# Optimization experiments

Measured on AMD Instinct MI355X. Metric: run time of the kernel, lower is better.

Reference implementation:

```python
import jax, jax.numpy as jnp
import numpy as np

N_NODES = 20000
N_EDGES = 500000


def setup_inputs() -> dict:
    key = jax.random.key(0)
    ks = jax.random.split(key, 12)
    s = 0.05  # small init scale for numerical sanity
    return {
        "z": jax.random.normal(ks[0], (N_NODES, 64), jnp.float32),
        "edge_index": jax.random.randint(ks[1], (2, N_EDGES), 0, N_NODES, jnp.int64),
        "celline_feats": jax.random.normal(ks[2], (N_NODES, 4), jnp.float32),
        "esm_repr": jax.random.normal(ks[3], (N_NODES, 320), jnp.float32),
        "mlp_w1": jax.random.normal(ks[4], (4, 64), jnp.float32) * s,
        "mlp_b1": jnp.zeros((64,), jnp.float32),
        "mlp_w2": jax.random.normal(ks[5], (64, 32), jnp.float32) * s,
        "mlp_b2": jnp.zeros((32,), jnp.float32),
        "mlp_w3": jax.random.normal(ks[6], (32, 16), jnp.float32) * s,
        "mlp_b3": jnp.zeros((16,), jnp.float32),
        "fc1_w": jax.random.normal(ks[7], (800, 400), jnp.float32) * s,
        "fc1_b": jnp.zeros((400,), jnp.float32),
        "fc2_w": jax.random.normal(ks[8], (400, 200), jnp.float32) * s,
        "fc2_b": jnp.zeros((200,), jnp.float32),
        "fc3_w": jax.random.normal(ks[9], (200, 100), jnp.float32) * s,
        "fc3_b": jnp.zeros((100,), jnp.float32),
        "fc4_w": jax.random.normal(ks[10], (100, 1), jnp.float32) * s,
        "fc4_b": jnp.zeros((1,), jnp.float32),
    }


def reference(z, edge_index, celline_feats, esm_repr,
              mlp_w1, mlp_b1, mlp_w2, mlp_b2, mlp_w3, mlp_b3,
              fc1_w, fc1_b, fc2_w, fc2_b, fc3_w, fc3_b, fc4_w, fc4_b):
    # cell_line_spec_mlp: 4 -> 64 -> 32 -> 16 (relu, relu, linear)
    m = jax.nn.relu(celline_feats @ mlp_w1 + mlp_b1)
    m = jax.nn.relu(m @ mlp_w2 + mlp_b2)
    m = m @ mlp_w3 + mlp_b3                       # [N, 16]
    # augment node embeddings: [N, 64+16+320] = [N, 400]
    zc = jnp.concatenate([z, m, esm_repr], axis=1)
    # gather endpoints, concat pair features: [E, 800]
    x = jnp.concatenate([zc[edge_index[0]], zc[edge_index[1]]], axis=1)
    # classifier MLP (dropout = identity in eval mode)
    x = jax.nn.relu(x @ fc1_w + fc1_b)
    x = jax.nn.relu(x @ fc2_w + fc2_b)
    x = jax.nn.relu(x @ fc3_w + fc3_b)
    x = x @ fc4_w + fc4_b                          # [E, 1]
    return jnp.squeeze(x, axis=-1)                 # [E]
```

## Files before the change

kernel.cpp:

```cpp
#include <hip/hip_runtime.h>


using u16    = unsigned short;
using bf16x8 = __attribute__((ext_vector_type(8))) short;
using f32x4  = __attribute__((ext_vector_type(4))) float;
using f32x16 = __attribute__((ext_vector_type(16))) float;
using i32x4  = __attribute__((ext_vector_type(4))) int;

#define NN   20000
#define NNP  20032
#define KD   416
#define NE   500000

#define W1F_ELEMS (50*13*512)
#define W2F_ELEMS (7*26*512)
#define W3F_ELEMS (4*14*512)
#define F4_ELEMS  128
#define PREP_TOT  (W1F_ELEMS + W2F_ELEMS + W3F_ELEMS + F4_ELEMS)

#define ZC_BLOCKS   (NNP / 4)
#define PREP_BLOCKS ((PREP_TOT + 255) / 256)

__device__ __forceinline__ u16 f2bf(float f) {
  unsigned u = __float_as_uint(f);
  u += 0x7fffu + ((u >> 16) & 1u);
  return (u16)(u >> 16);
}

__device__ __forceinline__ int cvt_pk_bf16(float lo, float hi) {
  int r;
  asm("v_cvt_pk_bf16_f32 %0, %1, %2" : "=v"(r) : "v"(lo), "v"(hi));
  return r;
}

__device__ __forceinline__ void gl_lds16(const u16* g, u16* l) {
  __builtin_amdgcn_global_load_lds(
      (const __attribute__((address_space(1))) unsigned int*)g,
      (__attribute__((address_space(3))) unsigned int*)l, 16, 0, 0);
}

__global__ __launch_bounds__(256) void prep_fused(
    const float* __restrict__ z, const float* __restrict__ cell,
    const float* __restrict__ esm,
    const float* __restrict__ w1, const float* __restrict__ b1,
    const float* __restrict__ w2, const float* __restrict__ b2,
    const float* __restrict__ w3, const float* __restrict__ b3,
    u16* __restrict__ zc,
    const float* __restrict__ fc1, const float* __restrict__ fc1b,
    const float* __restrict__ fc2, const float* __restrict__ fc2b,
    const float* __restrict__ fc3, const float* __restrict__ fc3b,
    const float* __restrict__ fc4,
    u16* __restrict__ W1f, u16* __restrict__ W2f, u16* __restrict__ W3f,
    float* __restrict__ fc4wp)
{
  __shared__ float h1s[4][64];
  __shared__ float h2s[4][32];
  __shared__ float ms[4][16];

  if (blockIdx.x < ZC_BLOCKS) {
    int tid = threadIdx.x, g = tid >> 6, t = tid & 63;
    int i = blockIdx.x * 4 + g;
    bool real = (i < NN);
    float c0 = 0, c1 = 0, c2 = 0, c3 = 0;
    if (real) {
      c0 = cell[(size_t)i * 4 + 0]; c1 = cell[(size_t)i * 4 + 1];
      c2 = cell[(size_t)i * 4 + 2]; c3 = cell[(size_t)i * 4 + 3];
    }
    float h = b1[t] + c0 * w1[t] + c1 * w1[64 + t] + c2 * w1[128 + t] + c3 * w1[192 + t];
    h1s[g][t] = fmaxf(h, 0.f);
    __syncthreads();
    if (t < 32) {
      float acc = b2[t];
      #pragma unroll 8
      for (int j = 0; j < 64; j++) acc += h1s[g][j] * w2[j * 32 + t];
      h2s[g][t] = fmaxf(acc, 0.f);
    }
    __syncthreads();
    if (t < 16) {
      float acc = b3[t];
      #pragma unroll 8
      for (int j = 0; j < 32; j++) acc += h2s[g][j] * w3[j * 16 + t];
      ms[g][t] = acc;
    }
    __syncthreads();
    u16* row = zc + (size_t)i * KD;
    for (int k = t; k < KD; k += 64) {
      float v = 0.f;
      if (real) {
        if (k < 64)       v = z[(size_t)i * 64 + k];
        else if (k < 80)  v = ms[g][k - 64];
        else if (k < 400) v = esm[(size_t)i * 320 + (k - 80)];
        else if (k == 400) v = 1.0f;
      }
      row[k] = f2bf(v);
    }
    return;
  }

  int idx = (blockIdx.x - ZC_BLOCKS) * 256 + threadIdx.x;
  if (idx < W1F_ELEMS) {
    int j = idx & 7, l = (idx >> 3) & 63, t = idx >> 9;
    int kb = t % 13, g = t / 13;
    int n = g * 16 + (l & 15);
    int k = kb * 32 + (l >> 4) * 8 + j;
    float v = 0.f;
    if (k < 400) v = (n < 400) ? fc1[(size_t)k * 400 + n]
                               : fc1[(size_t)(400 + k) * 400 + (n - 400)];
    else if (k == 400 && n < 400) v = fc1b[n];
    W1f[idx] = f2bf(v);
  } else if (idx < W1F_ELEMS + W2F_ELEMS) {
    int r = idx - W1F_ELEMS;
    int j = r & 7, l = (r >> 3) & 63, t = r >> 9;
    int kb = t % 26, nt = t / 26;
    int n = nt * 32 + (l & 31);
    int k = kb * 16 + (l >> 5) * 8 + j;
    float v = 0.f;
    if (n < 200) {
      if (k < 400) v = fc2[(size_t)k * 200 + n];
      else if (k == 400) v = fc2b[n];
    }
    W2f[r] = f2bf(v);
  } else if (idx < W1F_ELEMS + W2F_ELEMS + W3F_ELEMS) {
    int r = idx - (W1F_ELEMS + W2F_ELEMS);
    int j = r & 7, l = (r >> 3) & 63, t = r >> 9;
    int kb = t % 14, nt = t / 14;
    int n = nt * 32 + (l & 31);
    int k = kb * 16 + (l >> 5) * 8 + j;
    float v = 0.f;
    if (n < 100) {
      if (k < 200) v = fc3[(size_t)k * 100 + n];
      else if (k == 200) v = fc3b[n];
    }
    W3f[r] = f2bf(v);
  } else if (idx < PREP_TOT) {
    int r = idx - (W1F_ELEMS + W2F_ELEMS + W3F_ELEMS);
    fc4wp[r] = (r < 100) ? fc4[r] : 0.f;
  }
}

__global__ __launch_bounds__(256) void node_gemm(
    const u16* __restrict__ zc, const u16* __restrict__ W1f,
    u16* __restrict__ PQ)
{
  int tid = threadIdx.x, w = tid >> 6, l = tid & 63, lm = l & 15, quad = l >> 4;
  int mbase = blockIdx.x * 128 + w * 32;

  int ra = mbase + lm;       if (ra > NNP - 1) ra = NNP - 1;
  int rb = mbase + 16 + lm;  if (rb > NNP - 1) rb = NNP - 1;
  bf16x8 a0[13], a1[13];
  const u16* arow0 = zc + (size_t)ra * KD + quad * 8;
  const u16* arow1 = zc + (size_t)rb * KD + quad * 8;
  #pragma unroll
  for (int kb = 0; kb < 13; kb++) {
    a0[kb] = *(const bf16x8*)(arow0 + kb * 32);
    a1[kb] = *(const bf16x8*)(arow1 + kb * 32);
  }

  for (int nt = 0; nt < 10; nt++) {
    int g = blockIdx.y * 10 + nt;
    int ncol = g * 16 + lm;
    const u16* bbase = W1f + ((size_t)g * 13 * 64 + l) * 8;
    f32x4 acc0 = {0.f, 0.f, 0.f, 0.f};
    f32x4 acc1 = {0.f, 0.f, 0.f, 0.f};
    #pragma unroll
    for (int kb = 0; kb < 13; kb++) {
      bf16x8 b = *(const bf16x8*)(bbase + (size_t)kb * 512);
      acc0 = __builtin_amdgcn_mfma_f32_16x16x32_bf16(a0[kb], b, acc0, 0, 0, 0);
      acc1 = __builtin_amdgcn_mfma_f32_16x16x32_bf16(a1[kb], b, acc1, 0, 0, 0);
    }
    #pragma unroll
    for (int r = 0; r < 4; r++) {
      int row0 = mbase + quad * 4 + r;
      int row1 = row0 + 16;
      if (row0 < NNP) PQ[(size_t)row0 * 800 + ncol] = f2bf(acc0[r]);
      if (row1 < NNP) PQ[(size_t)row1 * 800 + ncol] = f2bf(acc1[r]);
    }
  }
}

__global__ __launch_bounds__(256, 3) void edge_kernel(
    const u16* __restrict__ PQ, const u16* __restrict__ W2f,
    const u16* __restrict__ W3f, const float* __restrict__ fc4wp,
    const float* __restrict__ fc4b,
    const int* __restrict__ ei, float* __restrict__ out)
{
  __shared__ __align__(16) u16 wsm[2][26 * 512];

  int tid = threadIdx.x, w = tid >> 6, l = tid & 63;
  int c = l & 31, h = l >> 5;
  int e = blockIdx.x * 128 + w * 32 + c;
  int ec = e < NE ? e : NE - 1;
  int s = ei[ec], d = ei[NE + ec];
  const u16* prow = PQ + (size_t)s * 800 + h * 8;
  const u16* qrow = PQ + (size_t)d * 800 + 400 + h * 8;

  for (int kb = w; kb < 26; kb += 4)
    gl_lds16(W2f + ((size_t)kb * 64 + l) * 8, &wsm[0][kb * 512]);

  i32x4 h1i[25];
  #pragma unroll
  for (int kb = 0; kb < 25; kb++) {
    i32x4 pv = *(const i32x4*)(prow + kb * 16);
    i32x4 qv = *(const i32x4*)(qrow + kb * 16);
    i32x4 r;
    #pragma unroll
    for (int j2 = 0; j2 < 4; j2++) {
      unsigned pu = (unsigned)pv[j2], qu = (unsigned)qv[j2];
      float lo = __uint_as_float(pu << 16) + __uint_as_float(qu << 16);
      float hi = __uint_as_float(pu & 0xFFFF0000u) + __uint_as_float(qu & 0xFFFF0000u);
      r[j2] = cvt_pk_bf16(fmaxf(lo, 0.f), fmaxf(hi, 0.f));
    }
    h1i[kb] = r;
  }
  i32x4 bias1 = {0, 0, 0, 0};
  if (h == 0) bias1[0] = 0x3f80;

  __syncthreads();

  int p2[7][8];
  #pragma unroll
  for (int nt = 0; nt < 7; nt++) {
    int cur = nt & 1;
    if (nt < 6) {
      for (int kb = w; kb < 26; kb += 4)
        gl_lds16(W2f + (((size_t)(nt + 1) * 26 + kb) * 64 + l) * 8,
                 &wsm[cur ^ 1][kb * 512]);
    } else {
      for (int kb = w; kb < 14; kb += 4)
        gl_lds16(W3f + ((size_t)kb * 64 + l) * 8, &wsm[cur ^ 1][kb * 512]);
    }
    f32x16 acc = {0.f,0.f,0.f,0.f,0.f,0.f,0.f,0.f,0.f,0.f,0.f,0.f,0.f,0.f,0.f,0.f};
    __builtin_amdgcn_s_setprio(1);
    #pragma unroll
    for (int kb = 0; kb < 25; kb++) {
      bf16x8 a = *(const bf16x8*)&wsm[cur][kb * 512 + l * 8];
      acc = __builtin_amdgcn_mfma_f32_32x32x16_bf16(
          a, __builtin_bit_cast(bf16x8, h1i[kb]), acc, 0, 0, 0);
    }
    {
      bf16x8 a = *(const bf16x8*)&wsm[cur][25 * 512 + l * 8];
      acc = __builtin_amdgcn_mfma_f32_32x32x16_bf16(
          a, __builtin_bit_cast(bf16x8, bias1), acc, 0, 0, 0);
    }
    __builtin_amdgcn_s_setprio(0);
    #pragma unroll
    for (int q = 0; q < 8; q++)
      p2[nt][q] = cvt_pk_bf16(fmaxf(acc[2 * q], 0.f), fmaxf(acc[2 * q + 1], 0.f));
    __syncthreads();
  }

  i32x4 b2f[14];
  #pragma unroll
  for (int kb3 = 0; kb3 < 14; kb3++) {
    int nt = kb3 >> 1;
    i32x4 f;
    #pragma unroll
    for (int jj = 0; jj < 4; jj++) {
      int q0 = (jj & 1) + 4 * (kb3 & 1);
      if (jj < 2) {
        int x = __shfl_xor(p2[nt][q0 + 2], 32);
        f[jj] = h ? x : p2[nt][q0];
      } else {
        int y = __shfl_xor(p2[nt][q0], 32);
        f[jj] = h ? p2[nt][q0 + 2] : y;
      }
    }
    if (kb3 == 12 && h) f[0] |= 0x3f80;
    b2f[kb3] = f;
  }

  float osum = 0.f;
  #pragma unroll
  for (int nt3 = 0; nt3 < 4; nt3++) {
    int cur = (7 + nt3) & 1;
    if (nt3 < 3) {
      for (int kb = w; kb < 14; kb += 4)
        gl_lds16(W3f + (((size_t)(nt3 + 1) * 14 + kb) * 64 + l) * 8,
                 &wsm[cur ^ 1][kb * 512]);
    }
    f32x16 acc = {0.f,0.f,0.f,0.f,0.f,0.f,0.f,0.f,0.f,0.f,0.f,0.f,0.f,0.f,0.f,0.f};
    __builtin_amdgcn_s_setprio(1);
    #pragma unroll
    for (int kb3 = 0; kb3 < 14; kb3++) {
      bf16x8 a = *(const bf16x8*)&wsm[cur][kb3 * 512 + l * 8];
      acc = __builtin_amdgcn_mfma_f32_32x32x16_bf16(
          a, __builtin_bit_cast(bf16x8, b2f[kb3]), acc, 0, 0, 0);
    }
    __builtin_amdgcn_s_setprio(0);
    #pragma unroll
    for (int r = 0; r < 16; r++) {
      int rho = (r & 3) + 8 * (r >> 2) + 4 * h + 32 * nt3;
      osum += fmaxf(acc[r], 0.f) * fc4wp[rho];
    }
    if (nt3 < 3) __syncthreads();
  }
  osum += __shfl_xor(osum, 32);
  if (h == 0 && e < NE) out[e] = osum + fc4b[0];
}

extern "C" void kernel_launch(void* const* d_in, const int* in_sizes, int n_in,
                              void* d_out, int out_size, void* d_ws, size_t ws_size,
                              hipStream_t stream) {
  (void)in_sizes; (void)n_in; (void)out_size; (void)ws_size;
  const float* z    = (const float*)d_in[0];
  const int*   ei   = (const int*)d_in[1];
  const float* cell = (const float*)d_in[2];
  const float* esm  = (const float*)d_in[3];
  const float* w1   = (const float*)d_in[4];
  const float* b1   = (const float*)d_in[5];
  const float* w2   = (const float*)d_in[6];
  const float* b2   = (const float*)d_in[7];
  const float* w3   = (const float*)d_in[8];
  const float* b3   = (const float*)d_in[9];
  const float* fc1w = (const float*)d_in[10];
  const float* fc1b = (const float*)d_in[11];
  const float* fc2w = (const float*)d_in[12];
  const float* fc2b = (const float*)d_in[13];
  const float* fc3w = (const float*)d_in[14];
  const float* fc3b = (const float*)d_in[15];
  const float* fc4w = (const float*)d_in[16];
  const float* fc4b = (const float*)d_in[17];
  float* out = (float*)d_out;

  u16* zc  = (u16*)d_ws;
  u16* PQ  = zc  + (size_t)NNP * KD;
  u16* W1f = PQ  + (size_t)NNP * 800;
  u16* W2f = W1f + W1F_ELEMS;
  u16* W3f = W2f + W2F_ELEMS;
  float* fc4wp = (float*)(W3f + W3F_ELEMS);

  prep_fused<<<ZC_BLOCKS + PREP_BLOCKS, 256, 0, stream>>>(
      z, cell, esm, w1, b1, w2, b2, w3, b3, zc,
      fc1w, fc1b, fc2w, fc2b, fc3w, fc3b, fc4w, W1f, W2f, W3f, fc4wp);
  node_gemm<<<dim3((NNP + 127) / 128, 5), 256, 0, stream>>>(zc, W1f, PQ);
  edge_kernel<<<(NE + 127) / 128, 256, 0, stream>>>(PQ, W2f, W3f, fc4wp, fc4b, ei, out);
}
```

Measured before the change: 359.2 us.

## Switch activations and weights from bf16 to fp16 with packed add-relu

Converts all stored activations and weights from bf16 to fp16 and uses fp16 MFMA instructions. The edge gather now does its add and relu with packed v_pk_add_f16/v_pk_max_f16, replacing the per-element unpack/add/convert sequence. The layer-3 K loop drops its all-zero 14th block, and edge_kernel occupancy is lowered from 3 to 2 waves per SIMD so the compiler gets more registers. fp16 has a narrower range than bf16, so large activations could overflow, and fewer resident waves reduces latency hiding.

Measured after the change: 356.8 us. Within noise of the previous version (-0.7%).

```diff
diff --git a/kernel.cpp b/kernel.cpp
--- a/kernel.cpp
+++ b/kernel.cpp
@@ -2,7 +2,8 @@
 
 
 using u16    = unsigned short;
-using bf16x8 = __attribute__((ext_vector_type(8))) short;
+using f16    = _Float16;
+using f16x8  = __attribute__((ext_vector_type(8))) f16;
 using f32x4  = __attribute__((ext_vector_type(4))) float;
 using f32x16 = __attribute__((ext_vector_type(16))) float;
 using i32x4  = __attribute__((ext_vector_type(4))) int;
@@ -21,15 +22,22 @@
 #define ZC_BLOCKS   (NNP / 4)
 #define PREP_BLOCKS ((PREP_TOT + 255) / 256)
 
-__device__ __forceinline__ u16 f2bf(float f) {
-  unsigned u = __float_as_uint(f);
-  u += 0x7fffu + ((u >> 16) & 1u);
-  return (u16)(u >> 16);
-}
-
-__device__ __forceinline__ int cvt_pk_bf16(float lo, float hi) {
+__device__ __forceinline__ u16 f2h(float f) {
+  f16 h = (f16)f;
+  return __builtin_bit_cast(u16, h);
+}
+
+__device__ __forceinline__ int cvt_pk_f16(float lo, float hi) {
   int r;
-  asm("v_cvt_pk_bf16_f32 %0, %1, %2" : "=v"(r) : "v"(lo), "v"(hi));
+  asm("v_cvt_pkrtz_f16_f32 %0, %1, %2" : "=v"(r) : "v"(lo), "v"(hi));
+  return r;
+}
+
+__device__ __forceinline__ int pk_addrelu(int p, int q) {
+  int r;
+  asm("v_pk_add_f16 %0, %1, %2\n\t"
+      "v_pk_max_f16 %0, %0, 0"
+      : "=&v"(r) : "v"(p), "v"(q));
   return r;
 }
 
@@ -92,7 +100,7 @@
         else if (k < 400) v = esm[(size_t)i * 320 + (k - 80)];
         else if (k == 400) v = 1.0f;
       }
-      row[k] = f2bf(v);
+      row[k] = f2h(v);
     }
     return;
   }
@@ -107,7 +115,7 @@
     if (k < 400) v = (n < 400) ? fc1[(size_t)k * 400 + n]
                                : fc1[(size_t)(400 + k) * 400 + (n - 400)];
     else if (k == 400 && n < 400) v = fc1b[n];
-    W1f[idx] = f2bf(v);
+    W1f[idx] = f2h(v);
   } else if (idx < W1F_ELEMS + W2F_ELEMS) {
     int r = idx - W1F_ELEMS;
     int j = r & 7, l = (r >> 3) & 63, t = r >> 9;
@@ -119,7 +127,7 @@
       if (k < 400) v = fc2[(size_t)k * 200 + n];
       else if (k == 400) v = fc2b[n];
     }
-    W2f[r] = f2bf(v);
+    W2f[r] = f2h(v);
   } else if (idx < W1F_ELEMS + W2F_ELEMS + W3F_ELEMS) {
     int r = idx - (W1F_ELEMS + W2F_ELEMS);
     int j = r & 7, l = (r >> 3) & 63, t = r >> 9;
@@ -131,7 +139,7 @@
       if (k < 200) v = fc3[(size_t)k * 100 + n];
       else if (k == 200) v = fc3b[n];
     }
-    W3f[r] = f2bf(v);
+    W3f[r] = f2h(v);
   } else if (idx < PREP_TOT) {
     int r = idx - (W1F_ELEMS + W2F_ELEMS + W3F_ELEMS);
     fc4wp[r] = (r < 100) ? fc4[r] : 0.f;
@@ -147,13 +155,13 @@
 
   int ra = mbase + lm;       if (ra > NNP - 1) ra = NNP - 1;
   int rb = mbase + 16 + lm;  if (rb > NNP - 1) rb = NNP - 1;
-  bf16x8 a0[13], a1[13];
+  f16x8 a0[13], a1[13];
   const u16* arow0 = zc + (size_t)ra * KD + quad * 8;
   const u16* arow1 = zc + (size_t)rb * KD + quad * 8;
   #pragma unroll
   for (int kb = 0; kb < 13; kb++) {
-    a0[kb] = *(const bf16x8*)(arow0 + kb * 32);
-    a1[kb] = *(const bf16x8*)(arow1 + kb * 32);
+    a0[kb] = *(const f16x8*)(arow0 + kb * 32);
+    a1[kb] = *(const f16x8*)(arow1 + kb * 32);
   }
 
   for (int nt = 0; nt < 10; nt++) {
@@ -164,21 +172,21 @@
     f32x4 acc1 = {0.f, 0.f, 0.f, 0.f};
     #pragma unroll
     for (int kb = 0; kb < 13; kb++) {
-      bf16x8 b = *(const bf16x8*)(bbase + (size_t)kb * 512);
-      acc0 = __builtin_amdgcn_mfma_f32_16x16x32_bf16(a0[kb], b, acc0, 0, 0, 0);
-      acc1 = __builtin_amdgcn_mfma_f32_16x16x32_bf16(a1[kb], b, acc1, 0, 0, 0);
+      f16x8 b = *(const f16x8*)(bbase + (size_t)kb * 512);
+      acc0 = __builtin_amdgcn_mfma_f32_16x16x32_f16(a0[kb], b, acc0, 0, 0, 0);
+      acc1 = __builtin_amdgcn_mfma_f32_16x16x32_f16(a1[kb], b, acc1, 0, 0, 0);
     }
     #pragma unroll
     for (int r = 0; r < 4; r++) {
       int row0 = mbase + quad * 4 + r;
       int row1 = row0 + 16;
-      if (row0 < NNP) PQ[(size_t)row0 * 800 + ncol] = f2bf(acc0[r]);
-      if (row1 < NNP) PQ[(size_t)row1 * 800 + ncol] = f2bf(acc1[r]);
-    }
-  }
-}
-
-__global__ __launch_bounds__(256, 3) void edge_kernel(
+      if (row0 < NNP) PQ[(size_t)row0 * 800 + ncol] = f2h(acc0[r]);
+      if (row1 < NNP) PQ[(size_t)row1 * 800 + ncol] = f2h(acc1[r]);
+    }
+  }
+}
+
+__global__ __launch_bounds__(256, 2) void edge_kernel(
     const u16* __restrict__ PQ, const u16* __restrict__ W2f,
     const u16* __restrict__ W3f, const float* __restrict__ fc4wp,
     const float* __restrict__ fc4b,
@@ -204,16 +212,11 @@
     i32x4 qv = *(const i32x4*)(qrow + kb * 16);
     i32x4 r;
     #pragma unroll
-    for (int j2 = 0; j2 < 4; j2++) {
-      unsigned pu = (unsigned)pv[j2], qu = (unsigned)qv[j2];
-      float lo = __uint_as_float(pu << 16) + __uint_as_float(qu << 16);
-      float hi = __uint_as_float(pu & 0xFFFF0000u) + __uint_as_float(qu & 0xFFFF0000u);
-      r[j2] = cvt_pk_bf16(fmaxf(lo, 0.f), fmaxf(hi, 0.f));
-    }
+    for (int j2 = 0; j2 < 4; j2++) r[j2] = pk_addrelu(pv[j2], qv[j2]);
     h1i[kb] = r;
   }
   i32x4 bias1 = {0, 0, 0, 0};
-  if (h == 0) bias1[0] = 0x3f80;
+  if (h == 0) bias1[0] = 0x3C00;
 
   __syncthreads();
 
@@ -226,32 +229,32 @@
         gl_lds16(W2f + (((size_t)(nt + 1) * 26 + kb) * 64 + l) * 8,
                  &wsm[cur ^ 1][kb * 512]);
     } else {
-      for (int kb = w; kb < 14; kb += 4)
+      for (int kb = w; kb < 13; kb += 4)
         gl_lds16(W3f + ((size_t)kb * 64 + l) * 8, &wsm[cur ^ 1][kb * 512]);
     }
     f32x16 acc = {0.f,0.f,0.f,0.f,0.f,0.f,0.f,0.f,0.f,0.f,0.f,0.f,0.f,0.f,0.f,0.f};
     __builtin_amdgcn_s_setprio(1);
     #pragma unroll
     for (int kb = 0; kb < 25; kb++) {
-      bf16x8 a = *(const bf16x8*)&wsm[cur][kb * 512 + l * 8];
-      acc = __builtin_amdgcn_mfma_f32_32x32x16_bf16(
-          a, __builtin_bit_cast(bf16x8, h1i[kb]), acc, 0, 0, 0);
+      f16x8 a = *(const f16x8*)&wsm[cur][kb * 512 + l * 8];
+      acc = __builtin_amdgcn_mfma_f32_32x32x16_f16(
+          a, __builtin_bit_cast(f16x8, h1i[kb]), acc, 0, 0, 0);
     }
     {
-      bf16x8 a = *(const bf16x8*)&wsm[cur][25 * 512 + l * 8];
-      acc = __builtin_amdgcn_mfma_f32_32x32x16_bf16(
-          a, __builtin_bit_cast(bf16x8, bias1), acc, 0, 0, 0);
+      f16x8 a = *(const f16x8*)&wsm[cur][25 * 512 + l * 8];
+      acc = __builtin_amdgcn_mfma_f32_32x32x16_f16(
+          a, __builtin_bit_cast(f16x8, bias1), acc, 0, 0, 0);
     }
     __builtin_amdgcn_s_setprio(0);
     #pragma unroll
     for (int q = 0; q < 8; q++)
-      p2[nt][q] = cvt_pk_bf16(fmaxf(acc[2 * q], 0.f), fmaxf(acc[2 * q + 1], 0.f));
+      p2[nt][q] = cvt_pk_f16(fmaxf(acc[2 * q], 0.f), fmaxf(acc[2 * q + 1], 0.f));
     __syncthreads();
   }
 
-  i32x4 b2f[14];
-  #pragma unroll
-  for (int kb3 = 0; kb3 < 14; kb3++) {
+  i32x4 b2f[13];
+  #pragma unroll
+  for (int kb3 = 0; kb3 < 13; kb3++) {
     int nt = kb3 >> 1;
     i32x4 f;
     #pragma unroll
@@ -265,7 +268,7 @@
         f[jj] = h ? p2[nt][q0 + 2] : y;
       }
     }
-    if (kb3 == 12 && h) f[0] |= 0x3f80;
+    if (kb3 == 12 && h) f[0] |= 0x3C00;
     b2f[kb3] = f;
   }
 
@@ -274,17 +277,17 @@
   for (int nt3 = 0; nt3 < 4; nt3++) {
     int cur = (7 + nt3) & 1;
     if (nt3 < 3) {
-      for (int kb = w; kb < 14; kb += 4)
+      for (int kb = w; kb < 13; kb += 4)
         gl_lds16(W3f + (((size_t)(nt3 + 1) * 14 + kb) * 64 + l) * 8,
                  &wsm[cur ^ 1][kb * 512]);
     }
     f32x16 acc = {0.f,0.f,0.f,0.f,0.f,0.f,0.f,0.f,0.f,0.f,0.f,0.f,0.f,0.f,0.f,0.f};
     __builtin_amdgcn_s_setprio(1);
     #pragma unroll
-    for (int kb3 = 0; kb3 < 14; kb3++) {
-      bf16x8 a = *(const bf16x8*)&wsm[cur][kb3 * 512 + l * 8];
-      acc = __builtin_amdgcn_mfma_f32_32x32x16_bf16(
-          a, __builtin_bit_cast(bf16x8, b2f[kb3]), acc, 0, 0, 0);
+    for (int kb3 = 0; kb3 < 13; kb3++) {
+      f16x8 a = *(const f16x8*)&wsm[cur][kb3 * 512 + l * 8];
+      acc = __builtin_amdgcn_mfma_f32_32x32x16_f16(
+          a, __builtin_bit_cast(f16x8, b2f[kb3]), acc, 0, 0, 0);
     }
     __builtin_amdgcn_s_setprio(0);
     #pragma unroll
```
